# Kernel tuning notes

Measured on AMD Instinct MI355X. Metric: run time of the kernel, lower is better.

## Reference

```python
import jax, jax.numpy as jnp
import numpy as np

EPS = 1e-7  # K.epsilon()
ROUTINGS = 3
NUM_CAPSULE = 32
DIM_CAPSULE = 64

def _squash(x, axis=-1):
    # NOTE: this repo's 'squash' is just L2-ish normalization: x / sqrt(||x||^2 + eps)
    s2 = jnp.sum(jnp.square(x), axis=axis, keepdims=True)
    return x / jnp.sqrt(s2 + EPS)

def setup_inputs() -> dict:
    key = jax.random.key(0)
    k1, k2 = jax.random.split(key)
    u_vecs = jax.random.normal(k1, (32, 1024, 256), dtype=jnp.float32)
    # shared-weight capsule kernel: (1, input_dim_capsule, num_capsule*dim_capsule)
    W = jax.random.normal(k2, (1, 256, NUM_CAPSULE * DIM_CAPSULE), dtype=jnp.float32) * 0.05
    return {"u_vecs": u_vecs, "W": W}

def reference(u_vecs, W):
    B, N, D = u_vecs.shape
    # conv1d with width-1 kernel == matmul over feature dim
    u_hat = jnp.einsum('bnd,dm->bnm', u_vecs, W[0])          # [B, N, NC*DC]
    u_hat = u_hat.reshape(B, N, NUM_CAPSULE, DIM_CAPSULE)
    u_hat = jnp.transpose(u_hat, (0, 2, 1, 3))               # [B, NC, N, DC]

    b = jnp.zeros((B, NUM_CAPSULE, N), dtype=u_hat.dtype)    # routing logits
    v = None
    for i in range(ROUTINGS):
        c = jax.nn.softmax(b, axis=-1)                       # over input capsules
        s = jnp.einsum('bij,bijd->bid', c, u_hat)            # weighted sum
        v = _squash(s)                                       # [B, NC, DC]
        if i < ROUTINGS - 1:
            b = b + jnp.einsum('bid,bijd->bij', v, u_hat)    # agreement update
    return v
```

## Files before the change

kernel.cpp:

```cpp
#include <hip/hip_runtime.h>
#include <math.h>


typedef short v8s __attribute__((ext_vector_type(8)));
typedef short v4s __attribute__((ext_vector_type(4)));
typedef short v2s __attribute__((ext_vector_type(2)));
typedef float v4f __attribute__((ext_vector_type(4)));

__device__ __forceinline__ unsigned short f2bf(float x) {
    unsigned u = __float_as_uint(x);
    u = u + 0x7fffu + ((u >> 16) & 1u);
    return (unsigned short)(u >> 16);
}
__device__ __forceinline__ float bf2f(unsigned short h) {
    return __uint_as_float(((unsigned)h) << 16);
}

__global__ __launch_bounds__(256) void k_init(const float* __restrict__ U,
                                              const float* __restrict__ W,
                                              float* __restrict__ t0p,
                                              float* __restrict__ WT) {
    int bid = blockIdx.x, tid = threadIdx.x;
    if (bid < 512) {
        int b = bid >> 4, q = bid & 15;
        const float* Up = U + (((b << 10) + (q << 6)) << 8) + tid;
        float acc = 0.f;
        #pragma unroll 16
        for (int jl = 0; jl < 64; ++jl) acc += Up[jl << 8];
        t0p[(b << 12) + (q << 8) + tid] = acc * (1.0f / 1024.0f);
    } else {
        __shared__ float tile[64 * 65];
        int tix = bid - 512;
        int k0 = (tix >> 5) << 6, c0 = (tix & 31) << 6;
        int cc = tid & 63, g4 = tid >> 6;
        #pragma unroll
        for (int r = 0; r < 16; ++r) {
            int kk = (g4 << 4) + r;
            tile[kk * 65 + cc] = W[(k0 + kk) * 2048 + c0 + cc];
        }
        __syncthreads();
        int kk = tid & 63;
        #pragma unroll
        for (int r = 0; r < 16; ++r) {
            int c = (g4 << 4) + r;
            WT[(c0 + c) * 256 + k0 + kk] = tile[kk * 65 + c];
        }
    }
}

__global__ __launch_bounds__(256) void k_sv(const float* __restrict__ t0p,
                                            const float* __restrict__ tpart,
                                            const float* __restrict__ sefpart,
                                            const float* __restrict__ W,
                                            const float* __restrict__ WT,
                                            short* __restrict__ wbt_h,
                                            short* __restrict__ wbt_l,
                                            float* __restrict__ out,
                                            int mode, int writeOut) {
    __shared__ float t_lds[256];
    __shared__ float spart[256];
    __shared__ __align__(16) float v_lds[64];
    __shared__ __align__(16) v4f spartw[256];
    __shared__ float sefv_s;
    int bid = blockIdx.x, tid = threadIdx.x;
    int b = bid >> 5, iG = bid & 31;
    int bg = (b << 1) | (iG >> 4), il = iG & 15;

    float acc = 0.f;
    if (mode == 0) {
        const float* tb = t0p + (b << 12) + tid;
        #pragma unroll
        for (int q = 0; q < 16; ++q) acc += tb[q << 8];
        if (tid == 0) sefv_s = 1.0f;
    } else {
        const float* tb = tpart + ((((bg << 4) + il)) << 8) + tid;
        #pragma unroll
        for (int p = 0; p < 8; ++p) acc += tb[p << 18];
        if (tid == 0) {
            float s = 0.f;
            #pragma unroll
            for (int p = 0; p < 8; ++p) s += sefpart[(((p << 6) + bg) << 4) + il];
            sefv_s = s;
        }
    }
    t_lds[tid] = acc;
    __syncthreads();

    int d = tid & 63, kq = tid >> 6;
    const float* Wc = W + ((kq << 6) * 2048) + (iG << 6) + d;
    float s = 0.f;
    #pragma unroll 4
    for (int kk = 0; kk < 64; ++kk)
        s += t_lds[(kq << 6) + kk] * Wc[kk * 2048];
    spart[tid] = s;
    __syncthreads();

    if (tid < 64) {
        float sv = spart[tid] + spart[tid + 64] + spart[tid + 128] + spart[tid + 192];
        float n2 = sv * sv;
        #pragma unroll
        for (int m = 1; m < 64; m <<= 1) n2 += __shfl_xor(n2, m, 64);
        float sf = sefv_s;
        float v = sv * rsqrtf(n2 + 1e-7f * sf * sf);
        v_lds[tid] = v;
        if (writeOut) out[(bid << 6) + tid] = v;
    }
    __syncthreads();
    if (writeOut) return;

    int k4 = tid & 63, dq = tid >> 6;
    const float4* WT4 = (const float4*)WT;
    v4f wp = {0.f, 0.f, 0.f, 0.f};
    #pragma unroll
    for (int dd = 0; dd < 16; ++dd) {
        float vv = v_lds[(dq << 4) + dd];
        float4 wt = WT4[((iG << 6) + (dq << 4) + dd) * 64 + k4];
        wp.x += vv * wt.x; wp.y += vv * wt.y; wp.z += vv * wt.z; wp.w += vv * wt.w;
    }
    spartw[(dq << 6) + k4] = wp;
    __syncthreads();
    if (tid < 64) {
        v4f w = spartw[tid] + spartw[64 + tid] + spartw[128 + tid] + spartw[192 + tid];
        float wv4[4] = {w.x, w.y, w.z, w.w};
        unsigned short wh[4], wl[4];
        #pragma unroll
        for (int e = 0; e < 4; ++e) {
            wh[e] = f2bf(wv4[e]);
            wl[e] = f2bf(wv4[e] - bf2f(wh[e]));
        }
        int base = (((bg << 4) + il) << 8) + (tid << 2);
        *(v4s*)&wbt_h[base] = (v4s){(short)wh[0], (short)wh[1], (short)wh[2], (short)wh[3]};
        *(v4s*)&wbt_l[base] = (v4s){(short)wl[0], (short)wl[1], (short)wl[2], (short)wl[3]};
    }
}

__global__ __launch_bounds__(1024, 8) void k_pass(const float* __restrict__ U,
                                                  const short* __restrict__ wbt_h,
                                                  const short* __restrict__ wbt_l,
                                                  float* __restrict__ bmatg,
                                                  float* __restrict__ tpart_out,
                                                  float* __restrict__ sefpart_out,
                                                  int addold) {
    __shared__ short s_stage[256 * 40];
    __shared__ short s_wh[16 * 264];
    __shared__ short s_wl[16 * 264];
    __shared__ short s_eh[16 * 136];
    __shared__ short s_el[16 * 136];
    __shared__ float s_sefp[8 * 16];

    const int tid = threadIdx.x, wv = tid >> 6, lane = tid & 63;
    const int quad = lane >> 4, nn = lane & 15;
    const int blk = blockIdx.x;
    const int b = blk & 31, pg = blk >> 5;
    const int p = pg >> 1, g2 = pg & 1;
    const int bg = (b << 1) | g2;
    const int rowbase = (b << 10) + (p << 7);
    const float4* U4 = (const float4*)U;

    if (tid < 512) {
        int row = tid >> 5, seg = tid & 31;
        int gidx = (((bg << 4) + row) << 8) + (seg << 3);
        *(v8s*)&s_wh[row * 264 + (seg << 3)] = *(const v8s*)(wbt_h + gidx);
        *(v8s*)&s_wl[row * 264 + (seg << 3)] = *(const v8s*)(wbt_l + gidx);
    }

    v4f dacc = {0.f, 0.f, 0.f, 0.f};
    const int jr = tid >> 3, ko = tid & 7;
    for (int kc = 0; kc < 8; ++kc) {
        __syncthreads();
        {
            float4 g = U4[(rowbase + jr) * 64 + (kc << 3) + ko];
            *(v4s*)&s_stage[jr * 32 + (ko << 2)] =
                (v4s){(short)f2bf(g.x), (short)f2bf(g.y),
                      (short)f2bf(g.z), (short)f2bf(g.w)};
        }
        __syncthreads();
        if (wv < 8) {
            v8s a  = *(const v8s*)&s_stage[((wv << 4) + nn) * 32 + (quad << 3)];
            v8s bh = *(const v8s*)&s_wh[nn * 264 + (kc << 5) + (quad << 3)];
            v8s bl = *(const v8s*)&s_wl[nn * 264 + (kc << 5) + (quad << 3)];
            dacc = __builtin_amdgcn_mfma_f32_16x16x32_bf16(a, bh, dacc, 0, 0, 0);
            dacc = __builtin_amdgcn_mfma_f32_16x16x32_bf16(a, bl, dacc, 0, 0, 0);
        }
    }
    if (wv < 8) {
        float sefl = 0.f;
        #pragma unroll
        for (int r = 0; r < 4; ++r) {
            int jloc = (wv << 4) + (quad << 2) + r;
            int ga = (((bg << 10) + (p << 7) + jloc) << 4) + nn;
            float logit = dacc[r];
            if (addold) logit += bmatg[ga];
            else bmatg[ga] = logit;
            float e = __expf(logit);
            sefl += e;
            unsigned short eh = f2bf(e);
            s_eh[nn * 136 + jloc] = (short)eh;
            s_el[nn * 136 + jloc] = (short)f2bf(e - bf2f(eh));
        }
        float se = sefl;
        se += __shfl_xor(se, 16, 64);
        se += __shfl_xor(se, 32, 64);
        if (lane < 16) s_sefp[(wv << 4) + lane] = se;
    }

    v4f tacc = {0.f, 0.f, 0.f, 0.f};
    const int j0 = wv << 1;
    for (int jc = 0; jc < 4; ++jc) {
        __syncthreads();
        {
            int r0 = (rowbase + (jc << 5) + j0) * 64 + lane;
            float4 g0 = U4[r0], g1 = U4[r0 + 64];
            float a0[4] = {g0.x, g0.y, g0.z, g0.w};
            float a1[4] = {g1.x, g1.y, g1.z, g1.w};
            #pragma unroll
            for (int e = 0; e < 4; ++e)
                *(v2s*)&s_stage[((lane << 2) + e) * 40 + j0] =
                    (v2s){(short)f2bf(a0[e]), (short)f2bf(a1[e])};
        }
        __syncthreads();
        v8s ah  = *(const v8s*)&s_stage[((wv << 4) + nn) * 40 + (quad << 3)];
        v8s beh = *(const v8s*)&s_eh[nn * 136 + (jc << 5) + (quad << 3)];
        v8s bel = *(const v8s*)&s_el[nn * 136 + (jc << 5) + (quad << 3)];
        tacc = __builtin_amdgcn_mfma_f32_16x16x32_bf16(ah, beh, tacc, 0, 0, 0);
        tacc = __builtin_amdgcn_mfma_f32_16x16x32_bf16(ah, bel, tacc, 0, 0, 0);
    }

    #pragma unroll
    for (int r = 0; r < 4; ++r) {
        int k = (wv << 4) + (quad << 2) + r;
        tpart_out[(((p << 6) + bg) << 12) + (nn << 8) + k] = tacc[r];
    }
    __syncthreads();
    if (tid < 16) {
        float ss = 0.f;
        #pragma unroll
        for (int w = 0; w < 8; ++w) ss += s_sefp[(w << 4) + tid];
        sefpart_out[(((p << 6) + bg) << 4) + tid] = ss;
    }
}

extern "C" void kernel_launch(void* const* d_in, const int* in_sizes, int n_in,
                              void* d_out, int out_size, void* d_ws, size_t ws_size,
                              hipStream_t stream) {
    const float* U = (const float*)d_in[0];
    const float* W = (const float*)d_in[1];
    float* out = (float*)d_out;
    float* ws = (float*)d_ws;

    float* t0p   = ws;
    float* WT    = t0p + 131072;
    float* bmatg = WT + 524288;
    float* tpA   = bmatg + 1048576;
    float* tpB   = tpA + 2097152;
    float* sefA  = tpB + 2097152;
    float* sefB  = sefA + 8192;
    short* wbt_h = (short*)(sefB + 8192);
    short* wbt_l = wbt_h + 262144;

    k_init<<<640, 256, 0, stream>>>(U, W, t0p, WT);
    k_sv<<<1024, 256, 0, stream>>>(t0p, nullptr, nullptr, W, WT,
                                   wbt_h, wbt_l, out, 0, 0);
    k_pass<<<512, 1024, 0, stream>>>(U, wbt_h, wbt_l, bmatg, tpA, sefA, 0);
    k_sv<<<1024, 256, 0, stream>>>(t0p, tpA, sefA, W, WT,
                                   wbt_h, wbt_l, out, 1, 0);
    k_pass<<<512, 1024, 0, stream>>>(U, wbt_h, wbt_l, bmatg, tpB, sefB, 1);
    k_sv<<<1024, 256, 0, stream>>>(t0p, tpB, sefB, W, WT,
                                   wbt_h, wbt_l, out, 1, 1);
}
```

Measured before the change: 141.7 us.

## Restructure routing pass to stage U tile once and split K across waves

The routing pass kernel now covers 64 input rows per block instead of 128 and launches twice as many blocks. Each block loads its whole U tile into LDS once, converted to bf16, and reuses it for both the logit GEMM and the weighted-sum GEMM. This replaces the repeated staging loops, with their per-chunk barriers and second global read of U. The logit GEMM splits K across all 16 waves and reduces the partials through LDS. The downstream reduction then sums 16 partials instead of 8, and both passes share a single partial buffer.

Result: faster. 131.4 us (-7.3%).

```diff
diff --git a/kernel.cpp b/kernel.cpp
--- a/kernel.cpp
+++ b/kernel.cpp
@@ -4,7 +4,6 @@
 
 typedef short v8s __attribute__((ext_vector_type(8)));
 typedef short v4s __attribute__((ext_vector_type(4)));
-typedef short v2s __attribute__((ext_vector_type(2)));
 typedef float v4f __attribute__((ext_vector_type(4)));
 
 __device__ __forceinline__ unsigned short f2bf(float x) {
@@ -73,13 +72,13 @@
         for (int q = 0; q < 16; ++q) acc += tb[q << 8];
         if (tid == 0) sefv_s = 1.0f;
     } else {
-        const float* tb = tpart + ((((bg << 4) + il)) << 8) + tid;
-        #pragma unroll
-        for (int p = 0; p < 8; ++p) acc += tb[p << 18];
+        const float* tb = tpart + (((bg << 4) + il) << 8) + tid;
+        #pragma unroll
+        for (int p = 0; p < 16; ++p) acc += tb[p << 18];
         if (tid == 0) {
             float s = 0.f;
             #pragma unroll
-            for (int p = 0; p < 8; ++p) s += sefpart[(((p << 6) + bg) << 4) + il];
+            for (int p = 0; p < 16; ++p) s += sefpart[(p << 10) + (bg << 4) + il];
             sefv_s = s;
         }
     }
@@ -141,12 +140,13 @@
                                                   float* __restrict__ tpart_out,
                                                   float* __restrict__ sefpart_out,
                                                   int addold) {
-    __shared__ short s_stage[256 * 40];
+    __shared__ short s_U[64 * 268];
     __shared__ short s_wh[16 * 264];
     __shared__ short s_wl[16 * 264];
-    __shared__ short s_eh[16 * 136];
-    __shared__ short s_el[16 * 136];
-    __shared__ float s_sefp[8 * 16];
+    __shared__ short s_eh[16 * 72];
+    __shared__ short s_el[16 * 72];
+    __shared__ float s_red[16 * 320];
+    __shared__ float s_sefp[16 * 16];
 
     const int tid = threadIdx.x, wv = tid >> 6, lane = tid & 63;
     const int quad = lane >> 4, nn = lane & 15;
@@ -154,8 +154,15 @@
     const int b = blk & 31, pg = blk >> 5;
     const int p = pg >> 1, g2 = pg & 1;
     const int bg = (b << 1) | g2;
-    const int rowbase = (b << 10) + (p << 7);
+    const int rowbase = (b << 10) + (p << 6);
     const float4* U4 = (const float4*)U;
+
+    const int mt2 = wv & 3, jq = wv >> 2;
+    const int rr = (jq << 2) + quad;
+    const int jloc = (mt2 << 4) + rr;
+    const int ga = (((bg << 10) + (p << 6) + jloc) << 4) + nn;
+    float bold = 0.f;
+    if (addold) bold = bmatg[ga];
 
     if (tid < 512) {
         int row = tid >> 5, seg = tid & 31;
@@ -163,80 +170,81 @@
         *(v8s*)&s_wh[row * 264 + (seg << 3)] = *(const v8s*)(wbt_h + gidx);
         *(v8s*)&s_wl[row * 264 + (seg << 3)] = *(const v8s*)(wbt_l + gidx);
     }
-
-    v4f dacc = {0.f, 0.f, 0.f, 0.f};
-    const int jr = tid >> 3, ko = tid & 7;
-    for (int kc = 0; kc < 8; ++kc) {
-        __syncthreads();
-        {
-            float4 g = U4[(rowbase + jr) * 64 + (kc << 3) + ko];
-            *(v4s*)&s_stage[jr * 32 + (ko << 2)] =
-                (v4s){(short)f2bf(g.x), (short)f2bf(g.y),
-                      (short)f2bf(g.z), (short)f2bf(g.w)};
-        }
-        __syncthreads();
-        if (wv < 8) {
-            v8s a  = *(const v8s*)&s_stage[((wv << 4) + nn) * 32 + (quad << 3)];
-            v8s bh = *(const v8s*)&s_wh[nn * 264 + (kc << 5) + (quad << 3)];
-            v8s bl = *(const v8s*)&s_wl[nn * 264 + (kc << 5) + (quad << 3)];
+    {
+        int col = tid & 63, row0 = tid >> 6;
+        float4 g[4];
+        #pragma unroll
+        for (int q = 0; q < 4; ++q)
+            g[q] = U4[(rowbase + row0 + (q << 4)) * 64 + col];
+        #pragma unroll
+        for (int q = 0; q < 4; ++q)
+            *(v4s*)&s_U[(row0 + (q << 4)) * 268 + (col << 2)] =
+                (v4s){(short)f2bf(g[q].x), (short)f2bf(g[q].y),
+                      (short)f2bf(g[q].z), (short)f2bf(g[q].w)};
+    }
+    __syncthreads();
+
+    {
+        const int mt = wv & 3, kq = wv >> 2;
+        v4f dacc = {0.f, 0.f, 0.f, 0.f};
+        #pragma unroll
+        for (int c = 0; c < 2; ++c) {
+            int kb = (kq << 6) + (c << 5) + (quad << 3);
+            v8s a  = *(const v8s*)&s_U[((mt << 4) + nn) * 268 + kb];
+            v8s bh = *(const v8s*)&s_wh[nn * 264 + kb];
+            v8s bl = *(const v8s*)&s_wl[nn * 264 + kb];
             dacc = __builtin_amdgcn_mfma_f32_16x16x32_bf16(a, bh, dacc, 0, 0, 0);
             dacc = __builtin_amdgcn_mfma_f32_16x16x32_bf16(a, bl, dacc, 0, 0, 0);
         }
-    }
-    if (wv < 8) {
-        float sefl = 0.f;
-        #pragma unroll
-        for (int r = 0; r < 4; ++r) {
-            int jloc = (wv << 4) + (quad << 2) + r;
-            int ga = (((bg << 10) + (p << 7) + jloc) << 4) + nn;
-            float logit = dacc[r];
-            if (addold) logit += bmatg[ga];
-            else bmatg[ga] = logit;
-            float e = __expf(logit);
-            sefl += e;
-            unsigned short eh = f2bf(e);
-            s_eh[nn * 136 + jloc] = (short)eh;
-            s_el[nn * 136 + jloc] = (short)f2bf(e - bf2f(eh));
-        }
-        float se = sefl;
+        #pragma unroll
+        for (int r = 0; r < 4; ++r)
+            s_red[wv * 320 + ((quad << 2) + r) * 20 + nn] = dacc[r];
+    }
+    __syncthreads();
+
+    {
+        float val = bold;
+        #pragma unroll
+        for (int kq = 0; kq < 4; ++kq)
+            val += s_red[((kq << 2) + mt2) * 320 + rr * 20 + nn];
+        if (!addold) bmatg[ga] = val;
+        float e = __expf(val);
+        unsigned short eh = f2bf(e);
+        s_eh[nn * 72 + jloc] = (short)eh;
+        s_el[nn * 72 + jloc] = (short)f2bf(e - bf2f(eh));
+        float se = e;
         se += __shfl_xor(se, 16, 64);
         se += __shfl_xor(se, 32, 64);
         if (lane < 16) s_sefp[(wv << 4) + lane] = se;
     }
-
-    v4f tacc = {0.f, 0.f, 0.f, 0.f};
-    const int j0 = wv << 1;
-    for (int jc = 0; jc < 4; ++jc) {
-        __syncthreads();
-        {
-            int r0 = (rowbase + (jc << 5) + j0) * 64 + lane;
-            float4 g0 = U4[r0], g1 = U4[r0 + 64];
-            float a0[4] = {g0.x, g0.y, g0.z, g0.w};
-            float a1[4] = {g1.x, g1.y, g1.z, g1.w};
+    __syncthreads();
+
+    {
+        v4f tacc = {0.f, 0.f, 0.f, 0.f};
+        const int k0 = wv << 4;
+        #pragma unroll
+        for (int jc = 0; jc < 2; ++jc) {
+            v8s aeh = *(const v8s*)&s_eh[nn * 72 + (jc << 5) + (quad << 3)];
+            v8s ael = *(const v8s*)&s_el[nn * 72 + (jc << 5) + (quad << 3)];
+            short bu[8];
             #pragma unroll
-            for (int e = 0; e < 4; ++e)
-                *(v2s*)&s_stage[((lane << 2) + e) * 40 + j0] =
-                    (v2s){(short)f2bf(a0[e]), (short)f2bf(a1[e])};
-        }
-        __syncthreads();
-        v8s ah  = *(const v8s*)&s_stage[((wv << 4) + nn) * 40 + (quad << 3)];
-        v8s beh = *(const v8s*)&s_eh[nn * 136 + (jc << 5) + (quad << 3)];
-        v8s bel = *(const v8s*)&s_el[nn * 136 + (jc << 5) + (quad << 3)];
-        tacc = __builtin_amdgcn_mfma_f32_16x16x32_bf16(ah, beh, tacc, 0, 0, 0);
-        tacc = __builtin_amdgcn_mfma_f32_16x16x32_bf16(ah, bel, tacc, 0, 0, 0);
-    }
-
-    #pragma unroll
-    for (int r = 0; r < 4; ++r) {
-        int k = (wv << 4) + (quad << 2) + r;
-        tpart_out[(((p << 6) + bg) << 12) + (nn << 8) + k] = tacc[r];
-    }
-    __syncthreads();
+            for (int jj = 0; jj < 8; ++jj)
+                bu[jj] = s_U[((jc << 5) + (quad << 3) + jj) * 268 + k0 + nn];
+            v8s bf = (v8s){bu[0], bu[1], bu[2], bu[3], bu[4], bu[5], bu[6], bu[7]};
+            tacc = __builtin_amdgcn_mfma_f32_16x16x32_bf16(aeh, bf, tacc, 0, 0, 0);
+            tacc = __builtin_amdgcn_mfma_f32_16x16x32_bf16(ael, bf, tacc, 0, 0, 0);
+        }
+        #pragma unroll
+        for (int r = 0; r < 4; ++r) {
+            int i = (quad << 2) + r;
+            tpart_out[(((((p << 6) + bg) << 4) + i) << 8) + k0 + nn] = tacc[r];
+        }
+    }
     if (tid < 16) {
         float ss = 0.f;
         #pragma unroll
-        for (int w = 0; w < 8; ++w) ss += s_sefp[(w << 4) + tid];
-        sefpart_out[(((p << 6) + bg) << 4) + tid] = ss;
+        for (int w = 0; w < 16; ++w) ss += s_sefp[(w << 4) + tid];
+        sefpart_out[(p << 10) + (bg << 4) + tid] = ss;
     }
 }
 
@@ -251,20 +259,18 @@
     float* t0p   = ws;
     float* WT    = t0p + 131072;
     float* bmatg = WT + 524288;
-    float* tpA   = bmatg + 1048576;
-    float* tpB   = tpA + 2097152;
-    float* sefA  = tpB + 2097152;
-    float* sefB  = sefA + 8192;
-    short* wbt_h = (short*)(sefB + 8192);
+    float* tp    = bmatg + 1048576;
+    float* sef   = tp + 4194304;
+    short* wbt_h = (short*)(sef + 16384);
     short* wbt_l = wbt_h + 262144;
 
     k_init<<<640, 256, 0, stream>>>(U, W, t0p, WT);
     k_sv<<<1024, 256, 0, stream>>>(t0p, nullptr, nullptr, W, WT,
                                    wbt_h, wbt_l, out, 0, 0);
-    k_pass<<<512, 1024, 0, stream>>>(U, wbt_h, wbt_l, bmatg, tpA, sefA, 0);
-    k_sv<<<1024, 256, 0, stream>>>(t0p, tpA, sefA, W, WT,
+    k_pass<<<1024, 1024, 0, stream>>>(U, wbt_h, wbt_l, bmatg, tp, sef, 0);
+    k_sv<<<1024, 256, 0, stream>>>(t0p, tp, sef, W, WT,
                                    wbt_h, wbt_l, out, 1, 0);
-    k_pass<<<512, 1024, 0, stream>>>(U, wbt_h, wbt_l, bmatg, tpB, sefB, 1);
-    k_sv<<<1024, 256, 0, stream>>>(t0p, tpB, sefB, W, WT,
+    k_pass<<<1024, 1024, 0, stream>>>(U, wbt_h, wbt_l, bmatg, tp, sef, 1);
+    k_sv<<<1024, 256, 0, stream>>>(t0p, tp, sef, W, WT,
                                    wbt_h, wbt_l, out, 1, 1);
 }
```
